# Performance work log

Hardware: AMD Instinct MI355X
Metric: run time of the kernel (lower is better)

The kernel has to match this reference:

```python
import jax, jax.numpy as jnp
import numpy as np

# SGCN (AsynSpiGCN) internals are not in the source; reconstructed as a standard
# LIF spiking-GCN: per time step, spikes propagate along edges weighted by
# edge_attr (gather src -> scatter-add dst), membrane potential decays with
# decay_alpha, neurons fire above threshold unless refractory, reset to v_r.
V_REST = 0.0
V_R = 0.0
SPEED = 1.0
THRESH = 0.5
REFRAC = 2.0
DECAY = 0.8
T_STEPS = 8
BETA = 0.5

N_NODES = 50000
N_EDGES = 800000
IN_DIM = 256
HID_DIM = 128


def setup_inputs() -> dict:
    key = jax.random.key(0)
    k1, k2, k3, k4, k5 = jax.random.split(key, 5)
    x = jax.random.normal(k1, (N_NODES, IN_DIM), dtype=jnp.float32)
    spike_node = jax.random.randint(k2, (N_NODES,), 0, 2, dtype=jnp.int32)
    edge_index = jax.random.randint(k3, (2, N_EDGES), 0, N_NODES, dtype=jnp.int32)
    node_indices = jnp.arange(N_NODES, dtype=jnp.int32)
    edge_attr = jax.random.uniform(k4, (N_EDGES,), dtype=jnp.float32)
    W = jax.random.normal(k5, (IN_DIM, HID_DIM), dtype=jnp.float32) * 0.05
    b = jnp.zeros((HID_DIM,), dtype=jnp.float32)
    return {"x": x, "spike_node": spike_node, "edge_index": edge_index,
            "node_indices": node_indices, "edge_attr": edge_attr, "W": W, "b": b}


def reference(x, spike_node, edge_index, node_indices, edge_attr, W, b):
    N = x.shape[0]
    # Linear projection + per-feature min-max standardization over nodes (dim 0)
    h = x @ W + b
    mn = h.min(axis=0, keepdims=True)
    mx = h.max(axis=0, keepdims=True)
    h = (h - mn) / (mx - mn + 1e-6)

    src, dst = edge_index[0], edge_index[1]
    v0 = jnp.full_like(h, V_REST)            # membrane potential [N, H]
    ref0 = jnp.zeros_like(h)                 # refractory counters [N, H]
    s0 = jnp.broadcast_to(spike_node.astype(h.dtype)[:, None], h.shape)

    def step(carry, _):
        v, ref, s = carry
        msg = s[src] * edge_attr[:, None]                      # [E, H] gather
        agg = jax.ops.segment_sum(msg, dst, num_segments=N)    # [N, H] scatter-add
        v = DECAY * v + SPEED * h + agg
        can_fire = ref <= 0
        spk = ((v >= THRESH) & can_fire).astype(h.dtype)
        v = jnp.where(spk > 0, V_R, v)
        ref = jnp.where(spk > 0, REFRAC, jnp.maximum(ref - 1.0, 0.0))
        return (v, ref, spk), spk

    (vT, _, _), spike_matrix = jax.lax.scan(step, (v0, ref0, s0), None, length=T_STEPS)
    fusion_tensor = h + BETA * vT
    return fusion_tensor, spike_matrix
```

## Files before the change

kernel.cpp:

```cpp
#include <hip/hip_runtime.h>
#include <cstdint>

#define N_NODES 50000
#define N_EDGES 800000
#define IN_DIM  256
#define HID     128
#define T_STEPS 8

#define AG_LOAD(p)     __hip_atomic_load((p), __ATOMIC_RELAXED, __HIP_MEMORY_SCOPE_AGENT)
#define AG_STORE(p, v) __hip_atomic_store((p), (v), __ATOMIC_RELAXED, __HIP_MEMORY_SCOPE_AGENT)
#define AG_ADD(p, v)   __hip_atomic_fetch_add((p), (v), __ATOMIC_RELAXED, __HIP_MEMORY_SCOPE_AGENT)
#define AG_MIN(p, v)   __hip_atomic_fetch_min((p), (v), __ATOMIC_RELAXED, __HIP_MEMORY_SCOPE_AGENT)
#define AG_MAX(p, v)   __hip_atomic_fetch_max((p), (v), __ATOMIC_RELAXED, __HIP_MEMORY_SCOPE_AGENT)

typedef unsigned long long u64;

static __device__ __forceinline__ unsigned int enc_f(float f) {
    unsigned int u = __float_as_uint(f);
    return (u & 0x80000000u) ? ~u : (u | 0x80000000u);
}
static __device__ __forceinline__ float dec_f(unsigned int u) {
    unsigned int b = (u & 0x80000000u) ? (u ^ 0x80000000u) : ~u;
    return __uint_as_float(b);
}

static __device__ __forceinline__ void fbar(int* bar, int nblk, int t) {
    int* flags = bar;
    int* go    = bar + 1900;
    __syncthreads();
    if (blockIdx.x == 0) {
        if (threadIdx.x == 0) AG_STORE(&flags[0], t);
        for (;;) {
            int ok = 1;
            for (int i = (int)threadIdx.x; i < nblk; i += 256)
                ok &= (AG_LOAD(&flags[i]) >= t);
            if (__syncthreads_and(ok)) break;
            __builtin_amdgcn_s_sleep(1);
        }
        if (threadIdx.x == 0) AG_STORE(go, t);
    } else {
        if (threadIdx.x == 0) {
            AG_STORE(&flags[blockIdx.x], t);
            while (AG_LOAD(go) < t) __builtin_amdgcn_s_sleep(4);
        }
        __syncthreads();
    }
}

template<int TNPB, int TNSLOT, int TECAP, int TMINW>
__global__ __launch_bounds__(256, TMINW) void k_mega(
    const float* __restrict__ x,
    const int*   __restrict__ spike_node,
    const int*   __restrict__ esrc,
    const int*   __restrict__ edst,
    const float* __restrict__ eattr,
    const float* __restrict__ W,
    const float* __restrict__ b,
    int* counts, int* cursor, int* row_ptr, int* blocksum,
    int4* edata4,
    unsigned int* mn_e, unsigned int* mx_e,
    uint32_t* sbA, uint32_t* sbB,
    float* __restrict__ out,
    int* bar, int nblk)
{
    __shared__ int      lrp[TNPB + 1];
    __shared__ uint32_t pool[TECAP * 6];
    __shared__ uint32_t sbw[TNPB][4];

    int*      ed_src_l  = (int*)pool;
    float*    ed_attr_l = (float*)(pool + TECAP);
    uint32_t* ed_wds    = pool + 2 * TECAP;
    float*    Ws        = (float*)pool;
    float*    xs        = (float*)(pool + 4096);
    float*    red_mn    = (float*)pool;
    float*    red_mx    = (float*)(pool + 1024);
    int*      rbuf      = (int*)pool;
    int*      cnt_l     = (int*)sbw;

    const int tid = threadIdx.x;
    const int bid = blockIdx.x;
    const int g   = tid >> 5, ln = tid & 31;
    const int n0  = bid * TNPB;
    const int ncnt = min(TNPB, N_NODES - n0);
    const int w = ln >> 3, shb = (ln & 7) * 4;
    const size_t NH = (size_t)N_NODES * HID;

    float4 hs[TNSLOT], vs[TNSLOT];
    uint32_t rcs[TNSLOT];
    #pragma unroll
    for (int s = 0; s < TNSLOT; ++s) hs[s] = make_float4(0.f, 0.f, 0.f, 0.f);
    int xoff[TNSLOT];
    #pragma unroll
    for (int s = 0; s < TNSLOT; ++s) xoff[s] = min(s * 8 + g, TNPB - 1) * 36;

    auto gemm_chunk = [&](int kc) {
        __syncthreads();
        for (int idx = tid; idx < TNPB * 8; idx += 256) {
            int node = idx >> 3, q = idx & 7;
            int row = min(n0 + node, N_NODES - 1);
            *(float4*)&xs[node * 36 + q * 4] =
                *(const float4*)(x + (size_t)row * IN_DIM + kc + q * 4);
        }
        for (int idx = tid; idx < 1024; idx += 256) {
            int r = idx >> 5, c = idx & 31;
            *(float4*)&Ws[r * 128 + c * 4] =
                *(const float4*)(W + (size_t)(kc + r) * HID + c * 4);
        }
        __syncthreads();
        #pragma unroll 4
        for (int k = 0; k < 32; ++k) {
            float4 wf = *(float4*)&Ws[k * 128 + ln * 4];
            #pragma unroll
            for (int s = 0; s < TNSLOT; ++s) {
                float xv = xs[xoff[s] + k];
                hs[s].x = __fmaf_rn(xv, wf.x, hs[s].x);
                hs[s].y = __fmaf_rn(xv, wf.y, hs[s].y);
                hs[s].z = __fmaf_rn(xv, wf.z, hs[s].z);
                hs[s].w = __fmaf_rn(xv, wf.w, hs[s].w);
            }
        }
    };

    for (int i = tid; i < ncnt; i += 256) AG_STORE(&counts[n0 + i], 0);
    if (bid == 0 && tid < HID) {
        AG_STORE(&mn_e[tid], 0xFFFFFFFFu);
        AG_STORE(&mx_e[tid], 0u);
    }
    fbar(bar, nblk, 1);

    for (int e = bid * 256 + tid; e < N_EDGES; e += nblk * 256)
        AG_ADD(&counts[edst[e]], 1);
    for (int kc = 0; kc < 128; kc += 32) gemm_chunk(kc);
    fbar(bar, nblk, 2);

    for (int i = tid; i < ncnt; i += 256) cnt_l[i] = AG_LOAD(&counts[n0 + i]);
    __syncthreads();
    if (tid == 0) {
        int s = 0;
        for (int i = 0; i < ncnt; ++i) s += cnt_l[i];
        AG_STORE(&blocksum[bid], s);
    }
    fbar(bar, nblk, 3);

    {
        int part = 0;
        for (int j = tid; j < bid; j += 256) part += AG_LOAD(&blocksum[j]);
        rbuf[tid] = part;
        __syncthreads();
        for (int off = 128; off > 0; off >>= 1) {
            if (tid < off) rbuf[tid] += rbuf[tid + off];
            __syncthreads();
        }
        if (tid == 0) {
            int run = rbuf[0];
            for (int i = 0; i < ncnt; ++i) { lrp[i] = run; run += cnt_l[i]; }
            lrp[ncnt] = run;
        }
        __syncthreads();
        for (int i = tid; i <= ncnt; i += 256) AG_STORE(&row_ptr[n0 + i], lrp[i]);
        for (int i = tid; i < ncnt; i += 256) AG_STORE(&cursor[n0 + i], lrp[i]);
    }
    fbar(bar, nblk, 4);

    for (int e = bid * 256 + tid; e < N_EDGES; e += nblk * 256) {
        int d = edst[e];
        int p = AG_ADD(&cursor[d], 1);
        u64 a  = (u64)(unsigned int)e | ((u64)(unsigned int)esrc[e] << 32);
        u64 bq = (u64)__float_as_uint(eattr[e]);
        u64* qp = (u64*)&edata4[p];
        AG_STORE(qp, a);
        AG_STORE(qp + 1, bq);
    }
    for (int kc = 128; kc < 256; kc += 32) gemm_chunk(kc);

    {
        float4 bv = *(const float4*)(b + ln * 4);
        float lmn[4], lmx[4];
        #pragma unroll
        for (int c = 0; c < 4; ++c) { lmn[c] = INFINITY; lmx[c] = -INFINITY; }
        #pragma unroll
        for (int s = 0; s < TNSLOT; ++s) {
            hs[s].x = __fadd_rn(hs[s].x, bv.x);
            hs[s].y = __fadd_rn(hs[s].y, bv.y);
            hs[s].z = __fadd_rn(hs[s].z, bv.z);
            hs[s].w = __fadd_rn(hs[s].w, bv.w);
            lmn[0] = fminf(lmn[0], hs[s].x); lmx[0] = fmaxf(lmx[0], hs[s].x);
            lmn[1] = fminf(lmn[1], hs[s].y); lmx[1] = fmaxf(lmx[1], hs[s].y);
            lmn[2] = fminf(lmn[2], hs[s].z); lmx[2] = fmaxf(lmx[2], hs[s].z);
            lmn[3] = fminf(lmn[3], hs[s].w); lmx[3] = fmaxf(lmx[3], hs[s].w);
        }
        __syncthreads();
        #pragma unroll
        for (int c = 0; c < 4; ++c) {
            red_mn[g * 128 + ln * 4 + c] = lmn[c];
            red_mx[g * 128 + ln * 4 + c] = lmx[c];
        }
        __syncthreads();
        if (tid < 128) {
            float mnv = red_mn[tid], mxv = red_mx[tid];
            #pragma unroll
            for (int r = 1; r < 8; ++r) {
                mnv = fminf(mnv, red_mn[r * 128 + tid]);
                mxv = fmaxf(mxv, red_mx[r * 128 + tid]);
            }
            AG_MIN(&mn_e[tid], enc_f(mnv));
            AG_MAX(&mx_e[tid], enc_f(mxv));
        }
        __syncthreads();
    }
    fbar(bar, nblk, 5);

    const int ebase = lrp[0];
    const int etot  = lrp[ncnt] - ebase;
    const bool inlds = (etot <= TECAP);

    for (int i = tid; i < ncnt; i += 256) {
        uint32_t f = spike_node[n0 + i] ? 0xFFFFFFFFu : 0u;
        u64 ff = (u64)f | ((u64)f << 32);
        AG_STORE((u64*)&sbA[(size_t)(n0 + i) * 4], ff);
        AG_STORE((u64*)&sbA[(size_t)(n0 + i) * 4 + 2], ff);
    }
    {
        float mn0 = dec_f(AG_LOAD(&mn_e[ln * 4 + 0]));
        float mn1 = dec_f(AG_LOAD(&mn_e[ln * 4 + 1]));
        float mn2 = dec_f(AG_LOAD(&mn_e[ln * 4 + 2]));
        float mn3 = dec_f(AG_LOAD(&mn_e[ln * 4 + 3]));
        float dd0 = __fadd_rn(__fsub_rn(dec_f(AG_LOAD(&mx_e[ln * 4 + 0])), mn0), 1e-6f);
        float dd1 = __fadd_rn(__fsub_rn(dec_f(AG_LOAD(&mx_e[ln * 4 + 1])), mn1), 1e-6f);
        float dd2 = __fadd_rn(__fsub_rn(dec_f(AG_LOAD(&mx_e[ln * 4 + 2])), mn2), 1e-6f);
        float dd3 = __fadd_rn(__fsub_rn(dec_f(AG_LOAD(&mx_e[ln * 4 + 3])), mn3), 1e-6f);
        #pragma unroll
        for (int s = 0; s < TNSLOT; ++s) {
            hs[s].x = __fdiv_rn(__fsub_rn(hs[s].x, mn0), dd0);
            hs[s].y = __fdiv_rn(__fsub_rn(hs[s].y, mn1), dd1);
            hs[s].z = __fdiv_rn(__fsub_rn(hs[s].z, mn2), dd2);
            hs[s].w = __fdiv_rn(__fsub_rn(hs[s].w, mn3), dd3);
        }
    }
    #pragma unroll
    for (int s = 0; s < TNSLOT; ++s) { vs[s] = make_float4(0.f,0.f,0.f,0.f); rcs[s] = 0u; }

    if (inlds) {
        for (int m = tid >> 6; m < ncnt; m += 4) {
            int l = tid & 63;
            int gbeg = lrp[m], lbeg = gbeg - ebase;
            int cnt = lrp[m + 1] - gbeg;
            if (cnt <= 0) continue;
            if (cnt <= 64) {
                int key = 0x7FFFFFFF, sv = 0, av = 0;
                if (l < cnt) {
                    u64 a  = AG_LOAD((u64*)&edata4[gbeg + l]);
                    u64 bq = AG_LOAD((u64*)&edata4[gbeg + l] + 1);
                    key = (int)(unsigned int)a;
                    sv  = (int)(unsigned int)(a >> 32);
                    av  = (int)(unsigned int)bq;
                }
                #pragma unroll
                for (int k = 2; k <= 64; k <<= 1) {
                    for (int j = k >> 1; j > 0; j >>= 1) {
                        int pk2 = __shfl_xor(key, j);
                        int ps  = __shfl_xor(sv, j);
                        int pa  = __shfl_xor(av, j);
                        bool lower = (l & j) == 0;
                        bool asc   = (l & k) == 0;
                        bool take  = (lower == asc) ? (pk2 < key) : (pk2 > key);
                        if (take) { key = pk2; sv = ps; av = pa; }
                    }
                }
                if (l < cnt) {
                    ed_src_l[lbeg + l]  = sv;
                    ed_attr_l[lbeg + l] = __int_as_float(av);
                }
            } else {
                if (l == 0) {
                    for (int i = 1; i < cnt; ++i) {
                        u64 ka = AG_LOAD((u64*)&edata4[gbeg + i]);
                        u64 kb = AG_LOAD((u64*)&edata4[gbeg + i] + 1);
                        int ke = (int)(unsigned int)ka;
                        int mm = i - 1;
                        while (mm >= 0) {
                            u64 ma = AG_LOAD((u64*)&edata4[gbeg + mm]);
                            if ((int)(unsigned int)ma <= ke) break;
                            AG_STORE((u64*)&edata4[gbeg + mm + 1], ma);
                            AG_STORE((u64*)&edata4[gbeg + mm + 1] + 1,
                                     AG_LOAD((u64*)&edata4[gbeg + mm] + 1));
                            --mm;
                        }
                        AG_STORE((u64*)&edata4[gbeg + mm + 1], ka);
                        AG_STORE((u64*)&edata4[gbeg + mm + 1] + 1, kb);
                    }
                }
                for (int i = l; i < cnt; i += 64) {
                    u64 a  = AG_LOAD((u64*)&edata4[gbeg + i]);
                    u64 bq = AG_LOAD((u64*)&edata4[gbeg + i] + 1);
                    ed_src_l[lbeg + i]  = (int)(unsigned int)(a >> 32);
                    ed_attr_l[lbeg + i] = __uint_as_float((unsigned int)bq);
                }
            }
        }
    } else {
        for (int m = tid >> 6; m < ncnt; m += 4) {
            int l = tid & 63;
            int gbeg = lrp[m];
            int cnt = lrp[m + 1] - gbeg;
            if (cnt <= 1) continue;
            if (cnt <= 64) {
                int key = 0x7FFFFFFF, sv = 0, av = 0;
                if (l < cnt) {
                    u64 a  = AG_LOAD((u64*)&edata4[gbeg + l]);
                    u64 bq = AG_LOAD((u64*)&edata4[gbeg + l] + 1);
                    key = (int)(unsigned int)a;
                    sv  = (int)(unsigned int)(a >> 32);
                    av  = (int)(unsigned int)bq;
                }
                #pragma unroll
                for (int k = 2; k <= 64; k <<= 1) {
                    for (int j = k >> 1; j > 0; j >>= 1) {
                        int pk2 = __shfl_xor(key, j);
                        int ps  = __shfl_xor(sv, j);
                        int pa  = __shfl_xor(av, j);
                        bool lower = (l & j) == 0;
                        bool asc   = (l & k) == 0;
                        bool take  = (lower == asc) ? (pk2 < key) : (pk2 > key);
                        if (take) { key = pk2; sv = ps; av = pa; }
                    }
                }
                if (l < cnt) {
                    u64 a = (u64)(unsigned int)key | ((u64)(unsigned int)sv << 32);
                    AG_STORE((u64*)&edata4[gbeg + l], a);
                    AG_STORE((u64*)&edata4[gbeg + l] + 1, (u64)(unsigned int)av);
                }
            } else if (l == 0) {
                for (int i = 1; i < cnt; ++i) {
                    u64 ka = AG_LOAD((u64*)&edata4[gbeg + i]);
                    u64 kb = AG_LOAD((u64*)&edata4[gbeg + i] + 1);
                    int ke = (int)(unsigned int)ka;
                    int mm = i - 1;
                    while (mm >= 0) {
                        u64 ma = AG_LOAD((u64*)&edata4[gbeg + mm]);
                        if ((int)(unsigned int)ma <= ke) break;
                        AG_STORE((u64*)&edata4[gbeg + mm + 1], ma);
                        AG_STORE((u64*)&edata4[gbeg + mm + 1] + 1,
                                 AG_LOAD((u64*)&edata4[gbeg + mm] + 1));
                        --mm;
                    }
                    AG_STORE((u64*)&edata4[gbeg + mm + 1], ka);
                    AG_STORE((u64*)&edata4[gbeg + mm + 1] + 1, kb);
                }
            }
        }
    }
    for (int i = tid; i < ncnt * 2; i += 256) ((u64*)sbw)[i] = 0ull;
    fbar(bar, nblk, 6);

    for (int t = 0; t < T_STEPS; ++t) {
        const uint32_t* cur = (t & 1) ? sbB : sbA;
        uint32_t*       nxt = (t & 1) ? sbA : sbB;
        if (t > 0) fbar(bar, nblk, 6 + t);

        if (inlds) {
            for (int i = tid; i < etot; i += 256) {
                u64* sp = (u64*)&cur[(size_t)ed_src_l[i] * 4];
                u64 lo = AG_LOAD(sp);
                u64 hi = AG_LOAD(sp + 1);
                uint4 wv;
                wv.x = (uint32_t)lo; wv.y = (uint32_t)(lo >> 32);
                wv.z = (uint32_t)hi; wv.w = (uint32_t)(hi >> 32);
                *(uint4*)&ed_wds[i * 4] = wv;
            }
        }
        __syncthreads();

        #pragma unroll
        for (int s = 0; s < TNSLOT; ++s) {
            int m = s * 8 + g;
            if (m < ncnt) {
                float ag0 = 0.f, ag1 = 0.f, ag2 = 0.f, ag3 = 0.f;
                if (inlds) {
                    int lb = lrp[m] - ebase, le = lrp[m + 1] - ebase;
                    int i = lb;
                    for (; i + 4 <= le; i += 4) {
                        uint32_t u0 = ed_wds[(i+0) * 4 + w]; float a0 = ed_attr_l[i+0];
                        uint32_t u1 = ed_wds[(i+1) * 4 + w]; float a1 = ed_attr_l[i+1];
                        uint32_t u2 = ed_wds[(i+2) * 4 + w]; float a2 = ed_attr_l[i+2];
                        uint32_t u3 = ed_wds[(i+3) * 4 + w]; float a3 = ed_attr_l[i+3];
                        uint32_t b0 = (u0 >> shb) & 0xFu;
                        uint32_t b1 = (u1 >> shb) & 0xFu;
                        uint32_t b2 = (u2 >> shb) & 0xFu;
                        uint32_t b3 = (u3 >> shb) & 0xFu;
                        ag0 = __fadd_rn(ag0, (b0 & 1u) ? a0 : 0.f);
                        ag1 = __fadd_rn(ag1, (b0 & 2u) ? a0 : 0.f);
                        ag2 = __fadd_rn(ag2, (b0 & 4u) ? a0 : 0.f);
                        ag3 = __fadd_rn(ag3, (b0 & 8u) ? a0 : 0.f);
                        ag0 = __fadd_rn(ag0, (b1 & 1u) ? a1 : 0.f);
                        ag1 = __fadd_rn(ag1, (b1 & 2u) ? a1 : 0.f);
                        ag2 = __fadd_rn(ag2, (b1 & 4u) ? a1 : 0.f);
                        ag3 = __fadd_rn(ag3, (b1 & 8u) ? a1 : 0.f);
                        ag0 = __fadd_rn(ag0, (b2 & 1u) ? a2 : 0.f);
                        ag1 = __fadd_rn(ag1, (b2 & 2u) ? a2 : 0.f);
                        ag2 = __fadd_rn(ag2, (b2 & 4u) ? a2 : 0.f);
                        ag3 = __fadd_rn(ag3, (b2 & 8u) ? a2 : 0.f);
                        ag0 = __fadd_rn(ag0, (b3 & 1u) ? a3 : 0.f);
                        ag1 = __fadd_rn(ag1, (b3 & 2u) ? a3 : 0.f);
                        ag2 = __fadd_rn(ag2, (b3 & 4u) ? a3 : 0.f);
                        ag3 = __fadd_rn(ag3, (b3 & 8u) ? a3 : 0.f);
                    }
                    for (; i < le; ++i) {
                        uint32_t u = ed_wds[i * 4 + w];
                        float a = ed_attr_l[i];
                        uint32_t bits = (u >> shb) & 0xFu;
                        ag0 = __fadd_rn(ag0, (bits & 1u) ? a : 0.f);
                        ag1 = __fadd_rn(ag1, (bits & 2u) ? a : 0.f);
                        ag2 = __fadd_rn(ag2, (bits & 4u) ? a : 0.f);
                        ag3 = __fadd_rn(ag3, (bits & 8u) ? a : 0.f);
                    }
                } else {
                    int lb = lrp[m], le = lrp[m + 1];
                    for (int i = lb; i < le; ++i) {
                        u64 a  = AG_LOAD((u64*)&edata4[i]);
                        u64 bq = AG_LOAD((u64*)&edata4[i] + 1);
                        int srcn = (int)(unsigned int)(a >> 32);
                        float av = __uint_as_float((unsigned int)bq);
                        uint32_t u = AG_LOAD((uint32_t*)&cur[(size_t)srcn * 4 + w]);
                        uint32_t bits = (u >> shb) & 0xFu;
                        ag0 = __fadd_rn(ag0, (bits & 1u) ? av : 0.f);
                        ag1 = __fadd_rn(ag1, (bits & 2u) ? av : 0.f);
                        ag2 = __fadd_rn(ag2, (bits & 4u) ? av : 0.f);
                        ag3 = __fadd_rn(ag3, (bits & 8u) ? av : 0.f);
                    }
                }

                float hv[4] = {hs[s].x, hs[s].y, hs[s].z, hs[s].w};
                float vv[4] = {vs[s].x, vs[s].y, vs[s].z, vs[s].w};
                float ag[4] = {ag0, ag1, ag2, ag3};
                float vf[4], sf[4];
                uint32_t rcu = rcs[s], rcn = 0u, nib = 0u;
                #pragma unroll
                for (int q = 0; q < 4; ++q) {
                    float vn = __fadd_rn(__fadd_rn(__fmul_rn(0.8f, vv[q]), hv[q]), ag[q]);
                    uint32_t rc = (rcu >> (8 * q)) & 0xFFu;
                    bool spk = (vn >= 0.5f) && (rc == 0u);
                    vf[q] = spk ? 0.0f : vn;
                    sf[q] = spk ? 1.0f : 0.0f;
                    uint32_t rnew = spk ? 2u : (rc > 0u ? rc - 1u : 0u);
                    rcn |= rnew << (8 * q);
                    nib |= (spk ? 1u : 0u) << q;
                }
                vs[s] = make_float4(vf[0], vf[1], vf[2], vf[3]);
                rcs[s] = rcn;
                size_t idx = (size_t)(n0 + m) * HID + ln * 4;
                *(float4*)&out[NH + (size_t)t * NH + idx] =
                    make_float4(sf[0], sf[1], sf[2], sf[3]);
                if (t == T_STEPS - 1) {
                    *(float4*)&out[idx] = make_float4(
                        __fadd_rn(hv[0], __fmul_rn(0.5f, vf[0])),
                        __fadd_rn(hv[1], __fmul_rn(0.5f, vf[1])),
                        __fadd_rn(hv[2], __fmul_rn(0.5f, vf[2])),
                        __fadd_rn(hv[3], __fmul_rn(0.5f, vf[3])));
                }
                atomicOr(&sbw[m][w], nib << shb);
            }
        }
        __syncthreads();
        for (int i = tid; i < ncnt * 2; i += 256) {
            AG_STORE((u64*)&nxt[(size_t)n0 * 4] + i, ((u64*)sbw)[i]);
            ((u64*)sbw)[i] = 0ull;
        }
    }
}

__global__ void k_count(const int* __restrict__ dst, int* __restrict__ counts) {
    int e = blockIdx.x * blockDim.x + threadIdx.x;
    if (e < N_EDGES) atomicAdd(&counts[dst[e]], 1);
}

__global__ void k_scan1(const int* __restrict__ counts, int* __restrict__ row_tmp,
                        int* __restrict__ blocksum) {
    __shared__ int sh[256];
    int t = threadIdx.x, i = blockIdx.x * 256 + t;
    int c = (i < N_NODES) ? counts[i] : 0;
    sh[t] = c; __syncthreads();
    for (int off = 1; off < 256; off <<= 1) {
        int val = (t >= off) ? sh[t - off] : 0;
        __syncthreads();
        sh[t] += val;
        __syncthreads();
    }
    if (i < N_NODES) row_tmp[i] = sh[t] - c;
    if (t == 255) blocksum[blockIdx.x] = sh[255];
}

__global__ void k_scan2(const int* __restrict__ blocksum, int* __restrict__ blockoff,
                        int nb, int* __restrict__ row_ptr) {
    if (threadIdx.x == 0) {
        int acc = 0;
        for (int b = 0; b < nb; ++b) { blockoff[b] = acc; acc += blocksum[b]; }
        row_ptr[N_NODES] = acc;
    }
}

__global__ void k_scan3(const int* __restrict__ row_tmp, const int* __restrict__ blockoff,
                        int* __restrict__ row_ptr) {
    int i = blockIdx.x * blockDim.x + threadIdx.x;
    if (i < N_NODES) row_ptr[i] = row_tmp[i] + blockoff[i >> 8];
}

__global__ void k_fill(const int* __restrict__ dst, const int* __restrict__ src,
                       const float* __restrict__ attr,
                       const int* __restrict__ row_ptr, int* __restrict__ cursor,
                       int* __restrict__ eid, int2* __restrict__ edata) {
    int e = blockIdx.x * blockDim.x + threadIdx.x;
    if (e >= N_EDGES) return;
    int d = dst[e];
    int p = row_ptr[d] + atomicAdd(&cursor[d], 1);
    eid[p]   = e;
    edata[p] = make_int2(src[e], __float_as_int(attr[e]));
}

__global__ __launch_bounds__(256) void k_bsort(const int* __restrict__ row_ptr,
                                               int* __restrict__ eid,
                                               int2* __restrict__ edata) {
    int node = blockIdx.x * 4 + (threadIdx.x >> 6);
    int l = threadIdx.x & 63;
    int beg = row_ptr[node], end = row_ptr[node + 1], cnt = end - beg;
    if (cnt <= 1) return;
    if (cnt <= 64) {
        int key = 0x7FFFFFFF, sv = 0, av = 0;
        if (l < cnt) { key = eid[beg + l]; int2 d = edata[beg + l]; sv = d.x; av = d.y; }
        #pragma unroll
        for (int k = 2; k <= 64; k <<= 1) {
            for (int j = k >> 1; j > 0; j >>= 1) {
                int pk = __shfl_xor(key, j);
                int ps = __shfl_xor(sv, j);
                int pa = __shfl_xor(av, j);
                bool lower = (l & j) == 0;
                bool asc   = (l & k) == 0;
                bool take = ((lower == asc)) ? (pk < key) : (pk > key);
                if (take) { key = pk; sv = ps; av = pa; }
            }
        }
        if (l < cnt) { eid[beg + l] = key; edata[beg + l] = make_int2(sv, av); }
    } else if (l == 0) {
        for (int i = beg + 1; i < end; ++i) {
            int ke = eid[i]; int2 kd = edata[i];
            int m = i - 1;
            while (m >= beg && eid[m] > ke) {
                eid[m+1] = eid[m]; edata[m+1] = edata[m]; --m;
            }
            eid[m+1] = ke; edata[m+1] = kd;
        }
    }
}

__global__ __launch_bounds__(256) void k_gemm(const float* __restrict__ x,
                                              const float* __restrict__ W,
                                              const float* __restrict__ b,
                                              float* __restrict__ h,
                                              unsigned int* __restrict__ mn_e,
                                              unsigned int* __restrict__ mx_e) {
    __shared__ float Ws[32 * 128];
    __shared__ float xs[64 * 36];
    __shared__ float red_mn[8 * 128];
    __shared__ float red_mx[8 * 128];
    const int tid = threadIdx.x;
    const int n0 = blockIdx.x * 64;
    const int jt = tid & 31, nt = tid >> 5;
    const int j0 = jt * 4;

    float acc[8][4];
    #pragma unroll
    for (int a = 0; a < 8; ++a)
        #pragma unroll
        for (int c = 0; c < 4; ++c) acc[a][c] = 0.0f;

    const int ldn = tid >> 2;
    const int kq  = (tid & 3) * 8;
    const int xrow = (n0 + ldn < N_NODES) ? (n0 + ldn) : (N_NODES - 1);
    const float* xg = x + (size_t)xrow * IN_DIM;

    for (int kc = 0; kc < IN_DIM; kc += 32) {
        __syncthreads();
        float4 xa = *(const float4*)(xg + kc + kq);
        float4 xb = *(const float4*)(xg + kc + kq + 4);
        *(float4*)&xs[ldn * 36 + kq]     = xa;
        *(float4*)&xs[ldn * 36 + kq + 4] = xb;
        #pragma unroll
        for (int p = 0; p < 4; ++p) {
            int r = nt + p * 8;
            *(float4*)&Ws[r * 128 + j0] =
                *(const float4*)(W + (size_t)(kc + r) * HID + j0);
        }
        __syncthreads();
        const float* xbase = &xs[nt * 8 * 36];
        #pragma unroll 4
        for (int k = 0; k < 32; ++k) {
            float4 wf = *(const float4*)&Ws[k * 128 + j0];
            #pragma unroll
            for (int ni = 0; ni < 8; ++ni) {
                float xv = xbase[ni * 36 + k];
                acc[ni][0] = __fmaf_rn(xv, wf.x, acc[ni][0]);
                acc[ni][1] = __fmaf_rn(xv, wf.y, acc[ni][1]);
                acc[ni][2] = __fmaf_rn(xv, wf.z, acc[ni][2]);
                acc[ni][3] = __fmaf_rn(xv, wf.w, acc[ni][3]);
            }
        }
    }

    float4 bv = *(const float4*)(b + j0);
    float lmn[4], lmx[4];
    #pragma unroll
    for (int c = 0; c < 4; ++c) { lmn[c] = INFINITY; lmx[c] = -INFINITY; }
    #pragma unroll
    for (int ni = 0; ni < 8; ++ni) {
        acc[ni][0] = __fadd_rn(acc[ni][0], bv.x);
        acc[ni][1] = __fadd_rn(acc[ni][1], bv.y);
        acc[ni][2] = __fadd_rn(acc[ni][2], bv.z);
        acc[ni][3] = __fadd_rn(acc[ni][3], bv.w);
        #pragma unroll
        for (int c = 0; c < 4; ++c) {
            lmn[c] = fminf(lmn[c], acc[ni][c]);
            lmx[c] = fmaxf(lmx[c], acc[ni][c]);
        }
    }
    #pragma unroll
    for (int c = 0; c < 4; ++c) {
        red_mn[nt * 128 + j0 + c] = lmn[c];
        red_mx[nt * 128 + j0 + c] = lmx[c];
    }
    __syncthreads();
    if (tid < 128) {
        float mnv = red_mn[tid], mxv = red_mx[tid];
        #pragma unroll
        for (int r = 1; r < 8; ++r) {
            mnv = fminf(mnv, red_mn[r * 128 + tid]);
            mxv = fmaxf(mxv, red_mx[r * 128 + tid]);
        }
        atomicMin(&mn_e[tid], enc_f(mnv));
        atomicMax(&mx_e[tid], enc_f(mxv));
    }
    #pragma unroll
    for (int ni = 0; ni < 8; ++ni) {
        int n = n0 + nt * 8 + ni;
        if (n < N_NODES)
            *(float4*)&h[(size_t)n * HID + j0] =
                make_float4(acc[ni][0], acc[ni][1], acc[ni][2], acc[ni][3]);
    }
}

__global__ void k_init_bits(const int* __restrict__ spike_node, uint32_t* __restrict__ sb) {
    int n = blockIdx.x * blockDim.x + threadIdx.x;
    if (n >= N_NODES) return;
    uint32_t f = spike_node[n] ? 0xFFFFFFFFu : 0u;
    sb[(size_t)n * 4 + 0] = f;
    sb[(size_t)n * 4 + 1] = f;
    sb[(size_t)n * 4 + 2] = f;
    sb[(size_t)n * 4 + 3] = f;
}

__global__ __launch_bounds__(128) void k_step(const int* __restrict__ row_ptr,
                                              const int2* __restrict__ edata,
                                              const uint32_t* __restrict__ sb_cur,
                                              uint32_t* __restrict__ sb_nxt,
                                              float* __restrict__ h,
                                              float* __restrict__ v,
                                              unsigned char* __restrict__ refc,
                                              const unsigned int* __restrict__ mn_e,
                                              const unsigned int* __restrict__ mx_e,
                                              float* __restrict__ out_spk,
                                              float* __restrict__ out_fus,
                                              int t0, int is_last) {
    __shared__ float    attr_l[4][128];
    __shared__ uint32_t words_l[4][128][4];
    __shared__ uint32_t sbw[16];
    __shared__ int      rp[5];

    const int tid = threadIdx.x;
    const int ns = tid >> 5, ln = tid & 31;
    const int nb = blockIdx.x * 4;
    const int n  = nb + ns;

    if (tid < 16) sbw[tid] = 0;
    if (tid < 5)  rp[tid] = row_ptr[nb + tid];
    __syncthreads();

    const int beg = rp[ns], cnt = rp[ns + 1] - beg;
    int cmax = 0;
    #pragma unroll
    for (int q = 0; q < 4; ++q) cmax = max(cmax, rp[q + 1] - rp[q]);
    const int nchunk = (cmax + 127) >> 7;

    float agg0 = 0.f, agg1 = 0.f, agg2 = 0.f, agg3 = 0.f;
    const int w = ln >> 3, shb = (ln & 7) * 4;

    for (int ch = 0; ch < nchunk; ++ch) {
        int base = ch << 7;
        __syncthreads();
        #pragma unroll
        for (int rep = 0; rep < 4; ++rep) {
            int i = base + rep * 32 + ln;
            if (i < cnt) {
                int2 d = edata[beg + i];
                attr_l[ns][rep * 32 + ln] = __int_as_float(d.y);
                *(uint4*)&words_l[ns][rep * 32 + ln][0] =
                    *(const uint4*)&sb_cur[(size_t)d.x * 4];
            }
        }
        __syncthreads();
        int lim = min(128, cnt - base);
        for (int i = 0; i < lim; ++i) {
            uint32_t u = words_l[ns][i][w];
            float a = attr_l[ns][i];
            uint32_t bits = (u >> shb) & 0xFu;
            agg0 = __fadd_rn(agg0, (bits & 1u) ? a : 0.0f);
            agg1 = __fadd_rn(agg1, (bits & 2u) ? a : 0.0f);
            agg2 = __fadd_rn(agg2, (bits & 4u) ? a : 0.0f);
            agg3 = __fadd_rn(agg3, (bits & 8u) ? a : 0.0f);
        }
    }

    const size_t idx = (size_t)n * HID + ln * 4;
    float4 h4 = *(const float4*)&h[idx];
    if (t0) {
        const int jb = ln * 4;
        float hq[4] = {h4.x, h4.y, h4.z, h4.w};
        #pragma unroll
        for (int q = 0; q < 4; ++q) {
            float mn = dec_f(mn_e[jb + q]);
            float mx = dec_f(mx_e[jb + q]);
            float d2 = __fadd_rn(__fsub_rn(mx, mn), 1e-6f);
            hq[q] = __fdiv_rn(__fsub_rn(hq[q], mn), d2);
        }
        h4 = make_float4(hq[0], hq[1], hq[2], hq[3]);
        *(float4*)&h[idx] = h4;
    }
    float4 v4;
    unsigned int rcu;
    if (t0) { v4 = make_float4(0.f, 0.f, 0.f, 0.f); rcu = 0u; }
    else    { v4 = *(const float4*)&v[idx]; rcu = *(const unsigned int*)&refc[idx]; }

    float hv[4]  = {h4.x, h4.y, h4.z, h4.w};
    float vv[4]  = {v4.x, v4.y, v4.z, v4.w};
    float ag[4]  = {agg0, agg1, agg2, agg3};
    float vf[4], sf[4];
    unsigned int rcn = 0u, nib = 0u;
    #pragma unroll
    for (int q = 0; q < 4; ++q) {
        float vn = __fadd_rn(__fadd_rn(__fmul_rn(0.8f, vv[q]), hv[q]), ag[q]);
        unsigned int rc = (rcu >> (8 * q)) & 0xFFu;
        bool spk = (vn >= 0.5f) && (rc == 0u);
        vf[q] = spk ? 0.0f : vn;
        sf[q] = spk ? 1.0f : 0.0f;
        unsigned int rnew = spk ? 2u : (rc > 0u ? rc - 1u : 0u);
        rcn |= rnew << (8 * q);
        nib |= (spk ? 1u : 0u) << q;
    }
    *(float4*)&v[idx] = make_float4(vf[0], vf[1], vf[2], vf[3]);
    *(unsigned int*)&refc[idx] = rcn;
    *(float4*)&out_spk[idx] = make_float4(sf[0], sf[1], sf[2], sf[3]);
    if (is_last) {
        *(float4*)&out_fus[idx] = make_float4(
            __fadd_rn(hv[0], __fmul_rn(0.5f, vf[0])),
            __fadd_rn(hv[1], __fmul_rn(0.5f, vf[1])),
            __fadd_rn(hv[2], __fmul_rn(0.5f, vf[2])),
            __fadd_rn(hv[3], __fmul_rn(0.5f, vf[3])));
    }
    atomicOr(&sbw[ns * 4 + w], nib << shb);
    __syncthreads();
    if (tid < 16)
        sb_nxt[(size_t)(nb + (tid >> 2)) * 4 + (tid & 3)] = sbw[tid];
}

extern "C" void kernel_launch(void* const* d_in, const int* in_sizes, int n_in,
                              void* d_out, int out_size, void* d_ws, size_t ws_size,
                              hipStream_t stream) {
    const float* x          = (const float*)d_in[0];
    const int*   spike_node = (const int*)  d_in[1];
    const int*   edge_index = (const int*)  d_in[2];
    const float* edge_attr  = (const float*)d_in[4];
    const float* W          = (const float*)d_in[5];
    const float* b          = (const float*)d_in[6];
    float* out = (float*)d_out;

    const int* src = edge_index;
    const int* dst = edge_index + N_EDGES;

    char* wsp = (char*)d_ws;
    auto alloc = [&](size_t bytes) {
        char* p = wsp;
        wsp += (bytes + 255) & ~(size_t)255;
        return p;
    };
    float*         h        = (float*)        alloc((size_t)N_NODES * HID * 4);
    float*         v        = (float*)        alloc((size_t)N_NODES * HID * 4);
    unsigned char* refc     = (unsigned char*)alloc((size_t)N_NODES * HID);
    uint32_t*      sbA      = (uint32_t*)     alloc((size_t)N_NODES * 16);
    uint32_t*      sbB      = (uint32_t*)     alloc((size_t)N_NODES * 16);
    int*           counts   = (int*)          alloc((size_t)N_NODES * 4);
    int*           cursor   = (int*)          alloc((size_t)N_NODES * 4);
    int*           row_tmp  = (int*)          alloc((size_t)N_NODES * 4);
    int*           row_ptr  = (int*)          alloc((size_t)(N_NODES + 1) * 4);
    int*           blocksum = (int*)          alloc(1024 * 4);
    int*           blockoff = (int*)          alloc(1024 * 4);
    int*           eid      = (int*)          alloc((size_t)N_EDGES * 4);
    int2*          edata    = (int2*)         alloc((size_t)N_EDGES * 8);
    unsigned int*  mn_e     = (unsigned int*) alloc(HID * 4);
    unsigned int*  mx_e     = (unsigned int*) alloc(HID * 4);
    int*           barv     = (int*)          alloc(8192);

    int4* edata4 = (int4*)h;

    const int NB = (N_NODES + 255) / 256;
    const int EB = (N_EDGES + 255) / 256;
    const size_t NH = (size_t)N_NODES * HID;

    auto kM = k_mega<66, 9, 1536, 3>;
    int occM = 0;
    hipOccupancyMaxActiveBlocksPerMultiprocessor(&occM, kM, 256, 0);

    if (occM >= 3) {
        hipMemsetAsync(barv, 0x00, 8192, stream);
        const int grid = (N_NODES + 65) / 66;
        kM<<<grid, 256, 0, stream>>>(x, spike_node, src, dst, edge_attr, W, b,
                                     counts, cursor, row_ptr, blocksum,
                                     edata4, mn_e, mx_e, sbA, sbB,
                                     out, barv, grid);
        return;
    }

    hipMemsetAsync(counts, 0x00, (size_t)N_NODES * 4, stream);
    hipMemsetAsync(cursor, 0x00, (size_t)N_NODES * 4, stream);
    hipMemsetAsync(mn_e,   0xFF, HID * 4, stream);
    hipMemsetAsync(mx_e,   0x00, HID * 4, stream);
    hipMemsetAsync(barv,   0x00, 8192, stream);

    k_count<<<EB, 256, 0, stream>>>(dst, counts);
    k_scan1<<<NB, 256, 0, stream>>>(counts, row_tmp, blocksum);
    k_scan2<<<1, 64, 0, stream>>>(blocksum, blockoff, NB, row_ptr);
    k_scan3<<<NB, 256, 0, stream>>>(row_tmp, blockoff, row_ptr);
    k_fill<<<EB, 256, 0, stream>>>(dst, src, edge_attr, row_ptr, cursor, eid, edata);
    k_bsort<<<N_NODES / 4, 256, 0, stream>>>(row_ptr, eid, edata);
    k_gemm<<<(N_NODES + 63) / 64, 256, 0, stream>>>(x, W, b, h, mn_e, mx_e);
    k_init_bits<<<NB, 256, 0, stream>>>(spike_node, sbA);

    for (int t = 0; t < T_STEPS; ++t) {
        uint32_t* cur = (t & 1) ? sbB : sbA;
        uint32_t* nxt = (t & 1) ? sbA : sbB;
        k_step<<<N_NODES / 4, 128, 0, stream>>>(row_ptr, edata, cur, nxt,
                                                h, v, refc, mn_e, mx_e,
                                                out + NH + (size_t)t * NH,
                                                out, (t == 0) ? 1 : 0,
                                                (t == T_STEPS - 1) ? 1 : 0);
    }
}
```

Baseline: 623.8 us.

## Replace CSR build with fixed-capacity per-node buckets in persistent megakernel

```diff
diff --git a/kernel.cpp b/kernel.cpp
--- a/kernel.cpp
+++ b/kernel.cpp
@@ -47,8 +47,8 @@
     }
 }
 
-template<int TNPB, int TNSLOT, int TECAP, int TMINW>
-__global__ __launch_bounds__(256, TMINW) void k_mega(
+template<int TNPB, int TNSLOT, int TECAP, int TBCAP, int TMINW>
+__global__ __launch_bounds__(256, TMINW) void k_mega2(
     const float* __restrict__ x,
     const int*   __restrict__ spike_node,
     const int*   __restrict__ esrc,
@@ -56,8 +56,7 @@
     const float* __restrict__ eattr,
     const float* __restrict__ W,
     const float* __restrict__ b,
-    int* counts, int* cursor, int* row_ptr, int* blocksum,
-    int4* edata4,
+    int* cnt, int4* bucket,
     unsigned int* mn_e, unsigned int* mx_e,
     uint32_t* sbA, uint32_t* sbB,
     float* __restrict__ out,
@@ -74,7 +73,6 @@
     float*    xs        = (float*)(pool + 4096);
     float*    red_mn    = (float*)pool;
     float*    red_mx    = (float*)(pool + 1024);
-    int*      rbuf      = (int*)pool;
     int*      cnt_l     = (int*)sbw;
 
     const int tid = threadIdx.x;
@@ -85,15 +83,34 @@
     const int w = ln >> 3, shb = (ln & 7) * 4;
     const size_t NH = (size_t)N_NODES * HID;
 
+    for (int i = tid; i < ncnt; i += 256) {
+        uint32_t f = spike_node[n0 + i] ? 0xFFFFFFFFu : 0u;
+        u64 ff = (u64)f | ((u64)f << 32);
+        AG_STORE((u64*)&sbA[(size_t)(n0 + i) * 4], ff);
+        AG_STORE((u64*)&sbA[(size_t)(n0 + i) * 4 + 2], ff);
+    }
+
+    for (int e = bid * 256 + tid; e < N_EDGES; e += nblk * 256) {
+        int d = edst[e];
+        int p = AG_ADD(&cnt[d], 1);
+        if (p < TBCAP) {
+            u64* qp = (u64*)&bucket[(size_t)d * TBCAP + p];
+            u64 a  = (u64)(unsigned int)e | ((u64)(unsigned int)esrc[e] << 32);
+            u64 bq = (u64)__float_as_uint(eattr[e]);
+            AG_STORE(qp, a);
+            AG_STORE(qp + 1, bq);
+        }
+    }
+
     float4 hs[TNSLOT], vs[TNSLOT];
-    uint32_t rcs[TNSLOT];
+    uint32_t rcs[TNSLOT], nibs[TNSLOT];
     #pragma unroll
     for (int s = 0; s < TNSLOT; ++s) hs[s] = make_float4(0.f, 0.f, 0.f, 0.f);
     int xoff[TNSLOT];
     #pragma unroll
     for (int s = 0; s < TNSLOT; ++s) xoff[s] = min(s * 8 + g, TNPB - 1) * 36;
 
-    auto gemm_chunk = [&](int kc) {
+    for (int kc = 0; kc < IN_DIM; kc += 32) {
         __syncthreads();
         for (int idx = tid; idx < TNPB * 8; idx += 256) {
             int node = idx >> 3, q = idx & 7;
@@ -119,60 +136,7 @@
                 hs[s].w = __fmaf_rn(xv, wf.w, hs[s].w);
             }
         }
-    };
-
-    for (int i = tid; i < ncnt; i += 256) AG_STORE(&counts[n0 + i], 0);
-    if (bid == 0 && tid < HID) {
-        AG_STORE(&mn_e[tid], 0xFFFFFFFFu);
-        AG_STORE(&mx_e[tid], 0u);
-    }
-    fbar(bar, nblk, 1);
-
-    for (int e = bid * 256 + tid; e < N_EDGES; e += nblk * 256)
-        AG_ADD(&counts[edst[e]], 1);
-    for (int kc = 0; kc < 128; kc += 32) gemm_chunk(kc);
-    fbar(bar, nblk, 2);
-
-    for (int i = tid; i < ncnt; i += 256) cnt_l[i] = AG_LOAD(&counts[n0 + i]);
-    __syncthreads();
-    if (tid == 0) {
-        int s = 0;
-        for (int i = 0; i < ncnt; ++i) s += cnt_l[i];
-        AG_STORE(&blocksum[bid], s);
-    }
-    fbar(bar, nblk, 3);
-
-    {
-        int part = 0;
-        for (int j = tid; j < bid; j += 256) part += AG_LOAD(&blocksum[j]);
-        rbuf[tid] = part;
-        __syncthreads();
-        for (int off = 128; off > 0; off >>= 1) {
-            if (tid < off) rbuf[tid] += rbuf[tid + off];
-            __syncthreads();
-        }
-        if (tid == 0) {
-            int run = rbuf[0];
-            for (int i = 0; i < ncnt; ++i) { lrp[i] = run; run += cnt_l[i]; }
-            lrp[ncnt] = run;
-        }
-        __syncthreads();
-        for (int i = tid; i <= ncnt; i += 256) AG_STORE(&row_ptr[n0 + i], lrp[i]);
-        for (int i = tid; i < ncnt; i += 256) AG_STORE(&cursor[n0 + i], lrp[i]);
-    }
-    fbar(bar, nblk, 4);
-
-    for (int e = bid * 256 + tid; e < N_EDGES; e += nblk * 256) {
-        int d = edst[e];
-        int p = AG_ADD(&cursor[d], 1);
-        u64 a  = (u64)(unsigned int)e | ((u64)(unsigned int)esrc[e] << 32);
-        u64 bq = (u64)__float_as_uint(eattr[e]);
-        u64* qp = (u64*)&edata4[p];
-        AG_STORE(qp, a);
-        AG_STORE(qp + 1, bq);
-    }
-    for (int kc = 128; kc < 256; kc += 32) gemm_chunk(kc);
-
+    }
     {
         float4 bv = *(const float4*)(b + ln * 4);
         float lmn[4], lmx[4];
@@ -208,18 +172,20 @@
         }
         __syncthreads();
     }
-    fbar(bar, nblk, 5);
-
-    const int ebase = lrp[0];
-    const int etot  = lrp[ncnt] - ebase;
+
+    fbar(bar, nblk, 1);
+
+    if (tid < ncnt) cnt_l[tid] = min(AG_LOAD(&cnt[n0 + tid]), TBCAP);
+    __syncthreads();
+    if (tid == 0) {
+        int run = 0;
+        for (int i = 0; i < ncnt; ++i) { lrp[i] = run; run += cnt_l[i]; }
+        lrp[ncnt] = run;
+    }
+    __syncthreads();
+    const int etot  = lrp[ncnt];
     const bool inlds = (etot <= TECAP);
 
-    for (int i = tid; i < ncnt; i += 256) {
-        uint32_t f = spike_node[n0 + i] ? 0xFFFFFFFFu : 0u;
-        u64 ff = (u64)f | ((u64)f << 32);
-        AG_STORE((u64*)&sbA[(size_t)(n0 + i) * 4], ff);
-        AG_STORE((u64*)&sbA[(size_t)(n0 + i) * 4 + 2], ff);
-    }
     {
         float mn0 = dec_f(AG_LOAD(&mn_e[ln * 4 + 0]));
         float mn1 = dec_f(AG_LOAD(&mn_e[ln * 4 + 1]));
@@ -243,14 +209,15 @@
     if (inlds) {
         for (int m = tid >> 6; m < ncnt; m += 4) {
             int l = tid & 63;
-            int gbeg = lrp[m], lbeg = gbeg - ebase;
-            int cnt = lrp[m + 1] - gbeg;
-            if (cnt <= 0) continue;
-            if (cnt <= 64) {
+            int lbeg = lrp[m];
+            int c = lrp[m + 1] - lbeg;
+            if (c <= 0) continue;
+            const u64* brow = (const u64*)&bucket[(size_t)(n0 + m) * TBCAP];
+            if (c <= 64) {
                 int key = 0x7FFFFFFF, sv = 0, av = 0;
-                if (l < cnt) {
-                    u64 a  = AG_LOAD((u64*)&edata4[gbeg + l]);
-                    u64 bq = AG_LOAD((u64*)&edata4[gbeg + l] + 1);
+                if (l < c) {
+                    u64 a  = AG_LOAD(brow + 2 * l);
+                    u64 bq = AG_LOAD(brow + 2 * l + 1);
                     key = (int)(unsigned int)a;
                     sv  = (int)(unsigned int)(a >> 32);
                     av  = (int)(unsigned int)bq;
@@ -267,48 +234,41 @@
                         if (take) { key = pk2; sv = ps; av = pa; }
                     }
                 }
-                if (l < cnt) {
+                if (l < c) {
                     ed_src_l[lbeg + l]  = sv;
                     ed_attr_l[lbeg + l] = __int_as_float(av);
                 }
-            } else {
-                if (l == 0) {
-                    for (int i = 1; i < cnt; ++i) {
-                        u64 ka = AG_LOAD((u64*)&edata4[gbeg + i]);
-                        u64 kb = AG_LOAD((u64*)&edata4[gbeg + i] + 1);
-                        int ke = (int)(unsigned int)ka;
-                        int mm = i - 1;
-                        while (mm >= 0) {
-                            u64 ma = AG_LOAD((u64*)&edata4[gbeg + mm]);
-                            if ((int)(unsigned int)ma <= ke) break;
-                            AG_STORE((u64*)&edata4[gbeg + mm + 1], ma);
-                            AG_STORE((u64*)&edata4[gbeg + mm + 1] + 1,
-                                     AG_LOAD((u64*)&edata4[gbeg + mm] + 1));
-                            --mm;
-                        }
-                        AG_STORE((u64*)&edata4[gbeg + mm + 1], ka);
-                        AG_STORE((u64*)&edata4[gbeg + mm + 1] + 1, kb);
+            } else if (l == 0) {
+                for (int i = 0; i < c; ++i) {
+                    u64 a  = AG_LOAD(brow + 2 * i);
+                    u64 bq = AG_LOAD(brow + 2 * i + 1);
+                    int ke  = (int)(unsigned int)a;
+                    int svv = (int)(unsigned int)(a >> 32);
+                    int avv = (int)(unsigned int)bq;
+                    int mm = i - 1;
+                    while (mm >= 0 && (int)ed_wds[lbeg + mm] > ke) {
+                        ed_wds[lbeg + mm + 1]    = ed_wds[lbeg + mm];
+                        ed_src_l[lbeg + mm + 1]  = ed_src_l[lbeg + mm];
+                        ed_attr_l[lbeg + mm + 1] = ed_attr_l[lbeg + mm];
+                        --mm;
                     }
-                }
-                for (int i = l; i < cnt; i += 64) {
-                    u64 a  = AG_LOAD((u64*)&edata4[gbeg + i]);
-                    u64 bq = AG_LOAD((u64*)&edata4[gbeg + i] + 1);
-                    ed_src_l[lbeg + i]  = (int)(unsigned int)(a >> 32);
-                    ed_attr_l[lbeg + i] = __uint_as_float((unsigned int)bq);
+                    ed_wds[lbeg + mm + 1]    = (uint32_t)ke;
+                    ed_src_l[lbeg + mm + 1]  = svv;
+                    ed_attr_l[lbeg + mm + 1] = __int_as_float(avv);
                 }
             }
         }
     } else {
         for (int m = tid >> 6; m < ncnt; m += 4) {
             int l = tid & 63;
-            int gbeg = lrp[m];
-            int cnt = lrp[m + 1] - gbeg;
-            if (cnt <= 1) continue;
-            if (cnt <= 64) {
+            int c = lrp[m + 1] - lrp[m];
+            if (c <= 1) continue;
+            u64* brow = (u64*)&bucket[(size_t)(n0 + m) * TBCAP];
+            if (c <= 64) {
                 int key = 0x7FFFFFFF, sv = 0, av = 0;
-                if (l < cnt) {
-                    u64 a  = AG_LOAD((u64*)&edata4[gbeg + l]);
-                    u64 bq = AG_LOAD((u64*)&edata4[gbeg + l] + 1);
+                if (l < c) {
+                    u64 a  = AG_LOAD(brow + 2 * l);
+                    u64 bq = AG_LOAD(brow + 2 * l + 1);
                     key = (int)(unsigned int)a;
                     sv  = (int)(unsigned int)(a >> 32);
                     av  = (int)(unsigned int)bq;
@@ -325,38 +285,50 @@
                         if (take) { key = pk2; sv = ps; av = pa; }
                     }
                 }
-                if (l < cnt) {
+                if (l < c) {
                     u64 a = (u64)(unsigned int)key | ((u64)(unsigned int)sv << 32);
-                    AG_STORE((u64*)&edata4[gbeg + l], a);
-                    AG_STORE((u64*)&edata4[gbeg + l] + 1, (u64)(unsigned int)av);
+                    AG_STORE(brow + 2 * l, a);
+                    AG_STORE(brow + 2 * l + 1, (u64)(unsigned int)av);
                 }
             } else if (l == 0) {
-                for (int i = 1; i < cnt; ++i) {
-                    u64 ka = AG_LOAD((u64*)&edata4[gbeg + i]);
-                    u64 kb = AG_LOAD((u64*)&edata4[gbeg + i] + 1);
+                for (int i = 1; i < c; ++i) {
+                    u64 ka = AG_LOAD(brow + 2 * i);
+                    u64 kb = AG_LOAD(brow + 2 * i + 1);
                     int ke = (int)(unsigned int)ka;
                     int mm = i - 1;
                     while (mm >= 0) {
-                        u64 ma = AG_LOAD((u64*)&edata4[gbeg + mm]);
+                        u64 ma = AG_LOAD(brow + 2 * mm);
                         if ((int)(unsigned int)ma <= ke) break;
-                        AG_STORE((u64*)&edata4[gbeg + mm + 1], ma);
-                        AG_STORE((u64*)&edata4[gbeg + mm + 1] + 1,
-                                 AG_LOAD((u64*)&edata4[gbeg + mm] + 1));
+                        AG_STORE(brow + 2 * mm + 2, ma);
+                        AG_STORE(brow + 2 * mm + 3, AG_LOAD(brow + 2 * mm + 1));
                         --mm;
                     }
-                    AG_STORE((u64*)&edata4[gbeg + mm + 1], ka);
-                    AG_STORE((u64*)&edata4[gbeg + mm + 1] + 1, kb);
-                }
-            }
-        }
-    }
+                    AG_STORE(brow + 2 * mm + 2, ka);
+                    AG_STORE(brow + 2 * mm + 3, kb);
+                }
+            }
+        }
+    }
+    __syncthreads();
     for (int i = tid; i < ncnt * 2; i += 256) ((u64*)sbw)[i] = 0ull;
-    fbar(bar, nblk, 6);
 
     for (int t = 0; t < T_STEPS; ++t) {
         const uint32_t* cur = (t & 1) ? sbB : sbA;
         uint32_t*       nxt = (t & 1) ? sbA : sbB;
-        if (t > 0) fbar(bar, nblk, 6 + t);
+        if (t > 0) {
+            fbar(bar, nblk, 1 + t);
+            #pragma unroll
+            for (int s = 0; s < TNSLOT; ++s) {
+                int m = s * 8 + g;
+                if (m < ncnt) {
+                    uint32_t nb4 = nibs[s];
+                    size_t idx = (size_t)(n0 + m) * HID + ln * 4;
+                    *(float4*)&out[NH + (size_t)(t - 1) * NH + idx] = make_float4(
+                        (nb4 & 1u) ? 1.0f : 0.0f, (nb4 & 2u) ? 1.0f : 0.0f,
+                        (nb4 & 4u) ? 1.0f : 0.0f, (nb4 & 8u) ? 1.0f : 0.0f);
+                }
+            }
+        }
 
         if (inlds) {
             for (int i = tid; i < etot; i += 256) {
@@ -377,35 +349,8 @@
             if (m < ncnt) {
                 float ag0 = 0.f, ag1 = 0.f, ag2 = 0.f, ag3 = 0.f;
                 if (inlds) {
-                    int lb = lrp[m] - ebase, le = lrp[m + 1] - ebase;
-                    int i = lb;
-                    for (; i + 4 <= le; i += 4) {
-                        uint32_t u0 = ed_wds[(i+0) * 4 + w]; float a0 = ed_attr_l[i+0];
-                        uint32_t u1 = ed_wds[(i+1) * 4 + w]; float a1 = ed_attr_l[i+1];
-                        uint32_t u2 = ed_wds[(i+2) * 4 + w]; float a2 = ed_attr_l[i+2];
-                        uint32_t u3 = ed_wds[(i+3) * 4 + w]; float a3 = ed_attr_l[i+3];
-                        uint32_t b0 = (u0 >> shb) & 0xFu;
-                        uint32_t b1 = (u1 >> shb) & 0xFu;
-                        uint32_t b2 = (u2 >> shb) & 0xFu;
-                        uint32_t b3 = (u3 >> shb) & 0xFu;
-                        ag0 = __fadd_rn(ag0, (b0 & 1u) ? a0 : 0.f);
-                        ag1 = __fadd_rn(ag1, (b0 & 2u) ? a0 : 0.f);
-                        ag2 = __fadd_rn(ag2, (b0 & 4u) ? a0 : 0.f);
-                        ag3 = __fadd_rn(ag3, (b0 & 8u) ? a0 : 0.f);
-                        ag0 = __fadd_rn(ag0, (b1 & 1u) ? a1 : 0.f);
-                        ag1 = __fadd_rn(ag1, (b1 & 2u) ? a1 : 0.f);
-                        ag2 = __fadd_rn(ag2, (b1 & 4u) ? a1 : 0.f);
-                        ag3 = __fadd_rn(ag3, (b1 & 8u) ? a1 : 0.f);
-                        ag0 = __fadd_rn(ag0, (b2 & 1u) ? a2 : 0.f);
-                        ag1 = __fadd_rn(ag1, (b2 & 2u) ? a2 : 0.f);
-                        ag2 = __fadd_rn(ag2, (b2 & 4u) ? a2 : 0.f);
-                        ag3 = __fadd_rn(ag3, (b2 & 8u) ? a2 : 0.f);
-                        ag0 = __fadd_rn(ag0, (b3 & 1u) ? a3 : 0.f);
-                        ag1 = __fadd_rn(ag1, (b3 & 2u) ? a3 : 0.f);
-                        ag2 = __fadd_rn(ag2, (b3 & 4u) ? a3 : 0.f);
-                        ag3 = __fadd_rn(ag3, (b3 & 8u) ? a3 : 0.f);
-                    }
-                    for (; i < le; ++i) {
+                    int lb = lrp[m], le = lrp[m + 1];
+                    for (int i = lb; i < le; ++i) {
                         uint32_t u = ed_wds[i * 4 + w];
                         float a = ed_attr_l[i];
                         uint32_t bits = (u >> shb) & 0xFu;
@@ -415,10 +360,11 @@
                         ag3 = __fadd_rn(ag3, (bits & 8u) ? a : 0.f);
                     }
                 } else {
-                    int lb = lrp[m], le = lrp[m + 1];
-                    for (int i = lb; i < le; ++i) {
-                        u64 a  = AG_LOAD((u64*)&edata4[i]);
-                        u64 bq = AG_LOAD((u64*)&edata4[i] + 1);
+                    int c = lrp[m + 1] - lrp[m];
+                    const u64* brow = (const u64*)&bucket[(size_t)(n0 + m) * TBCAP];
+                    for (int i = 0; i < c; ++i) {
+                        u64 a  = AG_LOAD(brow + 2 * i);
+                        u64 bq = AG_LOAD(brow + 2 * i + 1);
                         int srcn = (int)(unsigned int)(a >> 32);
                         float av = __uint_as_float((unsigned int)bq);
                         uint32_t u = AG_LOAD((uint32_t*)&cur[(size_t)srcn * 4 + w]);
@@ -433,7 +379,7 @@
                 float hv[4] = {hs[s].x, hs[s].y, hs[s].z, hs[s].w};
                 float vv[4] = {vs[s].x, vs[s].y, vs[s].z, vs[s].w};
                 float ag[4] = {ag0, ag1, ag2, ag3};
-                float vf[4], sf[4];
+                float vf[4];
                 uint32_t rcu = rcs[s], rcn = 0u, nib = 0u;
                 #pragma unroll
                 for (int q = 0; q < 4; ++q) {
@@ -441,23 +387,13 @@
                     uint32_t rc = (rcu >> (8 * q)) & 0xFFu;
                     bool spk = (vn >= 0.5f) && (rc == 0u);
                     vf[q] = spk ? 0.0f : vn;
-                    sf[q] = spk ? 1.0f : 0.0f;
                     uint32_t rnew = spk ? 2u : (rc > 0u ? rc - 1u : 0u);
                     rcn |= rnew << (8 * q);
                     nib |= (spk ? 1u : 0u) << q;
                 }
                 vs[s] = make_float4(vf[0], vf[1], vf[2], vf[3]);
                 rcs[s] = rcn;
-                size_t idx = (size_t)(n0 + m) * HID + ln * 4;
-                *(float4*)&out[NH + (size_t)t * NH + idx] =
-                    make_float4(sf[0], sf[1], sf[2], sf[3]);
-                if (t == T_STEPS - 1) {
-                    *(float4*)&out[idx] = make_float4(
-                        __fadd_rn(hv[0], __fmul_rn(0.5f, vf[0])),
-                        __fadd_rn(hv[1], __fmul_rn(0.5f, vf[1])),
-                        __fadd_rn(hv[2], __fmul_rn(0.5f, vf[2])),
-                        __fadd_rn(hv[3], __fmul_rn(0.5f, vf[3])));
-                }
+                nibs[s] = nib;
                 atomicOr(&sbw[m][w], nib << shb);
             }
         }
@@ -465,6 +401,23 @@
         for (int i = tid; i < ncnt * 2; i += 256) {
             AG_STORE((u64*)&nxt[(size_t)n0 * 4] + i, ((u64*)sbw)[i]);
             ((u64*)sbw)[i] = 0ull;
+        }
+    }
+
+    #pragma unroll
+    for (int s = 0; s < TNSLOT; ++s) {
+        int m = s * 8 + g;
+        if (m < ncnt) {
+            uint32_t nb4 = nibs[s];
+            size_t idx = (size_t)(n0 + m) * HID + ln * 4;
+            *(float4*)&out[NH + (size_t)(T_STEPS - 1) * NH + idx] = make_float4(
+                (nb4 & 1u) ? 1.0f : 0.0f, (nb4 & 2u) ? 1.0f : 0.0f,
+                (nb4 & 4u) ? 1.0f : 0.0f, (nb4 & 8u) ? 1.0f : 0.0f);
+            *(float4*)&out[idx] = make_float4(
+                __fadd_rn(hs[s].x, __fmul_rn(0.5f, vs[s].x)),
+                __fadd_rn(hs[s].y, __fmul_rn(0.5f, vs[s].y)),
+                __fadd_rn(hs[s].z, __fmul_rn(0.5f, vs[s].z)),
+                __fadd_rn(hs[s].w, __fmul_rn(0.5f, vs[s].w)));
         }
     }
 }
@@ -790,6 +743,37 @@
         wsp += (bytes + 255) & ~(size_t)255;
         return p;
     };
+
+    const int NB = (N_NODES + 255) / 256;
+    const int EB = (N_EDGES + 255) / 256;
+    const size_t NH = (size_t)N_NODES * HID;
+    const int BCAP = 80;
+
+    auto kM = k_mega2<66, 9, 1536, 80, 3>;
+    int occM = 0;
+    hipOccupancyMaxActiveBlocksPerMultiprocessor(&occM, kM, 256, 0);
+
+    if (occM >= 3) {
+        int4*         bucket = (int4*)        alloc((size_t)N_NODES * BCAP * 16);
+        int*          cnt    = (int*)         alloc((size_t)N_NODES * 4);
+        uint32_t*     sbA    = (uint32_t*)    alloc((size_t)N_NODES * 16);
+        uint32_t*     sbB    = (uint32_t*)    alloc((size_t)N_NODES * 16);
+        unsigned int* mn_e   = (unsigned int*)alloc(HID * 4);
+        unsigned int* mx_e   = (unsigned int*)alloc(HID * 4);
+        int*          barv   = (int*)         alloc(8192);
+
+        hipMemsetAsync(cnt,  0x00, (size_t)N_NODES * 4, stream);
+        hipMemsetAsync(mn_e, 0xFF, HID * 4, stream);
+        hipMemsetAsync(mx_e, 0x00, HID * 4, stream);
+        hipMemsetAsync(barv, 0x00, 8192, stream);
+
+        const int grid = (N_NODES + 65) / 66;
+        kM<<<grid, 256, 0, stream>>>(x, spike_node, src, dst, edge_attr, W, b,
+                                     cnt, bucket, mn_e, mx_e, sbA, sbB,
+                                     out, barv, grid);
+        return;
+    }
+
     float*         h        = (float*)        alloc((size_t)N_NODES * HID * 4);
     float*         v        = (float*)        alloc((size_t)N_NODES * HID * 4);
     unsigned char* refc     = (unsigned char*)alloc((size_t)N_NODES * HID);
@@ -805,33 +789,11 @@
     int2*          edata    = (int2*)         alloc((size_t)N_EDGES * 8);
     unsigned int*  mn_e     = (unsigned int*) alloc(HID * 4);
     unsigned int*  mx_e     = (unsigned int*) alloc(HID * 4);
-    int*           barv     = (int*)          alloc(8192);
-
-    int4* edata4 = (int4*)h;
-
-    const int NB = (N_NODES + 255) / 256;
-    const int EB = (N_EDGES + 255) / 256;
-    const size_t NH = (size_t)N_NODES * HID;
-
-    auto kM = k_mega<66, 9, 1536, 3>;
-    int occM = 0;
-    hipOccupancyMaxActiveBlocksPerMultiprocessor(&occM, kM, 256, 0);
-
-    if (occM >= 3) {
-        hipMemsetAsync(barv, 0x00, 8192, stream);
-        const int grid = (N_NODES + 65) / 66;
-        kM<<<grid, 256, 0, stream>>>(x, spike_node, src, dst, edge_attr, W, b,
-                                     counts, cursor, row_ptr, blocksum,
-                                     edata4, mn_e, mx_e, sbA, sbB,
-                                     out, barv, grid);
-        return;
-    }
 
     hipMemsetAsync(counts, 0x00, (size_t)N_NODES * 4, stream);
     hipMemsetAsync(cursor, 0x00, (size_t)N_NODES * 4, stream);
     hipMemsetAsync(mn_e,   0xFF, HID * 4, stream);
     hipMemsetAsync(mx_e,   0x00, HID * 4, stream);
-    hipMemsetAsync(barv,   0x00, 8192, stream);
 
     k_count<<<EB, 256, 0, stream>>>(dst, counts);
     k_scan1<<<NB, 256, 0, stream>>>(counts, row_tmp, blocksum);
```

Measured after the change: 622.0 us. Within noise of the previous version (-0.3%).
